# Kernel tuning notes

Hardware: AMD Instinct MI355X
Metric: run time of the kernel (lower is better)

The kernel has to match this reference:

```python
import jax, jax.numpy as jnp
import numpy as np

HEADS = 4  # from init_kwargs

def setup_inputs() -> dict:
    key = jax.random.key(0)
    ks = jax.random.split(key, 11)
    B, N, T, E = 1, 16, 2048, 64
    D = E // HEADS
    return {
        "value": jax.random.normal(ks[0], (B, N, T, E), jnp.float32),
        "key":   jax.random.normal(ks[1], (B, N, T, E), jnp.float32),
        "query": jax.random.normal(ks[2], (B, N, T, E), jnp.float32),
        "Wq": jax.random.normal(ks[3], (D, D), jnp.float32) / np.sqrt(D),
        "bq": jax.random.normal(ks[4], (D,), jnp.float32) * 0.01,
        "Wk": jax.random.normal(ks[5], (D, D), jnp.float32) / np.sqrt(D),
        "bk": jax.random.normal(ks[6], (D,), jnp.float32) * 0.01,
        "Wv": jax.random.normal(ks[7], (D, D), jnp.float32) / np.sqrt(D),
        "bv": jax.random.normal(ks[8], (D,), jnp.float32) * 0.01,
        "Wfc": jax.random.normal(ks[9], (E, E), jnp.float32) / np.sqrt(E),
        "bfc": jax.random.normal(ks[10], (E,), jnp.float32) * 0.01,
    }

def reference(value, key, query, Wq, bq, Wk, bk, Wv, bv, Wfc, bfc):
    B, N, T, E = query.shape
    H = HEADS
    D = E // H
    # split heads: [B,N,T,H,D]
    q = query.reshape(B, N, T, H, D) @ Wq + bq
    k = key.reshape(B, N, T, H, D) @ Wk + bk
    v = value.reshape(B, N, T, H, D) @ Wv + bv
    # full score tensor [B,N,Tq,Tk,H]
    scores = jnp.einsum('bnqhd,bnkhd->bnqkh', q, k)
    # NOTE: original softmaxes over dim=2, i.e. the QUERY axis (faithful to source)
    attn = jax.nn.softmax(scores / jnp.float32(E) ** 0.5, axis=2)
    out = jnp.einsum('bnqkh,bnkhd->bnqhd', attn, v).reshape(B, N, T, E)
    return out @ Wfc + bfc
```

## Files before the change

kernel.cpp:

```cpp
#include <hip/hip_runtime.h>

#define N_ 16
#define T_ 2048
#define E_ 64
#define H_ 4
#define D_ 16
#define NH_ 64
#define SEXP_ 0.18033688f

typedef __attribute__((ext_vector_type(4))) _Float16 h4;
typedef __attribute__((ext_vector_type(8))) _Float16 h8;
typedef __attribute__((ext_vector_type(2))) __fp16 g2;
typedef __attribute__((ext_vector_type(4))) float f4;

#if __has_builtin(__builtin_amdgcn_exp2f)
__device__ inline float fast_exp2(float x) { return __builtin_amdgcn_exp2f(x); }
#else
__device__ inline float fast_exp2(float x) {
    float r; asm("v_exp_f32 %0, %1" : "=v"(r) : "v"(x)); return r;
}
#endif

__device__ inline h4 pack4_f16(float a, float b, float c, float d) {
    union { g2 g[2]; h4 h; } u;
    u.g[0] = __builtin_amdgcn_cvt_pkrtz(a, b);
    u.g[1] = __builtin_amdgcn_cvt_pkrtz(c, d);
    return u.h;
}

__global__ __launch_bounds__(256) void proj_kernel(
    const float* __restrict__ xq, const float* __restrict__ Wq, const float* __restrict__ bq,
    const float* __restrict__ xk, const float* __restrict__ Wk, const float* __restrict__ bk,
    const float* __restrict__ xv, const float* __restrict__ Wv, const float* __restrict__ bv,
    const float* __restrict__ Wfc,
    _Float16* __restrict__ Qh, _Float16* __restrict__ Kh, _Float16* __restrict__ Vt,
    _Float16* __restrict__ Wt)
{
    int tid = threadIdx.x;
    int y = blockIdx.y;
    if (y == 3) {
        if (blockIdx.x < 16) {
            int k = blockIdx.x * 4 + (tid >> 6);
            int e = tid & 63;
            Wt[e * 64 + k] = (_Float16)Wfc[k * 64 + e];
        }
        return;
    }
    const float* x = (y == 0) ? xq : (y == 1) ? xk : xv;
    const float* W = (y == 0) ? Wq : (y == 1) ? Wk : Wv;
    const float* b = (y == 0) ? bq : (y == 1) ? bk : bv;
    const float sc = (y == 0) ? SEXP_ : 1.0f;

    __shared__ float Wl[D_ * D_];
    __shared__ float bl[D_];
    Wl[tid] = W[tid];
    if (tid < D_) bl[tid] = b[tid];
    __syncthreads();

    int r = blockIdx.x * 256 + tid;
    int h, t, n;
    if (y == 2) {
        t = r & (T_ - 1);
        h = (r >> 11) & (H_ - 1);
        n = r >> 13;
    } else {
        h = r & (H_ - 1);
        t = (r >> 2) & (T_ - 1);
        n = r >> 13;
    }

    const float4* xp4 = reinterpret_cast<const float4*>(
        x + ((size_t)(n * T_ + t) * E_ + h * D_));
    float xv_[D_];
#pragma unroll
    for (int i = 0; i < 4; i++) {
        float4 v = xp4[i];
        xv_[4*i] = v.x; xv_[4*i+1] = v.y; xv_[4*i+2] = v.z; xv_[4*i+3] = v.w;
    }
    float acc[D_];
#pragma unroll
    for (int i = 0; i < D_; i++) acc[i] = bl[i];
#pragma unroll
    for (int j = 0; j < D_; j++) {
        float xj = xv_[j];
#pragma unroll
        for (int i = 0; i < D_; i++) acc[i] = fmaf(xj, Wl[j * D_ + i], acc[i]);
    }
    if (y == 2) {
        _Float16* vb = Vt + (size_t)(n * H_ + h) * D_ * T_ + t;
#pragma unroll
        for (int d = 0; d < D_; d++) vb[(size_t)d * T_] = (_Float16)acc[d];
    } else {
        _Float16 ob[16];
#pragma unroll
        for (int i = 0; i < D_; i++) ob[i] = (_Float16)(acc[i] * sc);
        _Float16* out = (y == 0) ? Qh : Kh;
        uint4* dst = reinterpret_cast<uint4*>(out + (size_t)((n * H_ + h) * T_ + t) * D_);
        dst[0] = reinterpret_cast<uint4*>(ob)[0];
        dst[1] = reinterpret_cast<uint4*>(ob)[1];
    }
}

__global__ __launch_bounds__(256) void stats_kernel(
    const _Float16* __restrict__ Qh, const _Float16* __restrict__ Kh,
    float* __restrict__ Lp)
{
    int tid = threadIdx.x;
    int lane = tid & 63, wave = tid >> 6;
    int row = lane & 15, quad = lane >> 4;
    int nh = blockIdx.x;
    int kt0 = (blockIdx.y * 4 + wave) * 4;
    int z = blockIdx.z;
    const _Float16* Kb = Kh + (size_t)nh * T_ * D_;
    const _Float16* Qb = Qh + (size_t)nh * T_ * D_;

    h4 a[4];
#pragma unroll
    for (int j = 0; j < 4; j++)
        a[j] = *reinterpret_cast<const h4*>(Kb + ((kt0 + j) * 16 + row) * D_ + quad * 4);

    f4 l[4];
#pragma unroll
    for (int j = 0; j < 4; j++) l[j] = (f4){0.f, 0.f, 0.f, 0.f};
    f4 z4 = {0.f, 0.f, 0.f, 0.f};

    int q_lo = z * (T_ / 4), q_hi = q_lo + T_ / 4;
#pragma unroll 4
    for (int q0 = q_lo; q0 < q_hi; q0 += 16) {
        h4 b = *reinterpret_cast<const h4*>(Qb + (q0 + row) * D_ + quad * 4);
#pragma unroll
        for (int j = 0; j < 4; j++) {
            f4 s = __builtin_amdgcn_mfma_f32_16x16x16f16(a[j], b, z4, 0, 0, 0);
#pragma unroll
            for (int i = 0; i < 4; i++) l[j][i] += fast_exp2(s[i]);
        }
    }
#pragma unroll
    for (int off = 1; off < 16; off <<= 1)
#pragma unroll
        for (int j = 0; j < 4; j++)
#pragma unroll
            for (int i = 0; i < 4; i++)
                l[j][i] += __shfl_xor(l[j][i], off, 64);

    if (row == 0) {
        float* lp = Lp + ((size_t)z * NH_ + nh) * T_;
#pragma unroll
        for (int j = 0; j < 4; j++)
            *reinterpret_cast<f4*>(lp + (kt0 + j) * 16 + quad * 4) = l[j];
    }
}

__global__ __launch_bounds__(256) void combine_kernel(
    const float* __restrict__ Lp, _Float16* __restrict__ Vt)
{
    int nh = blockIdx.x >> 1;
    int k0 = (blockIdx.x & 1) * 1024 + threadIdx.x * 4;

    f4 s = {0.f, 0.f, 0.f, 0.f};
#pragma unroll
    for (int zz = 0; zz < 4; zz++) {
        f4 lv = *reinterpret_cast<const f4*>(Lp + ((size_t)zz * NH_ + nh) * T_ + k0);
        s[0] += lv[0]; s[1] += lv[1]; s[2] += lv[2]; s[3] += lv[3];
    }
    f4 r;
#pragma unroll
    for (int i = 0; i < 4; i++) r[i] = 1.0f / s[i];

    _Float16* vb = Vt + (size_t)nh * D_ * T_ + k0;
#pragma unroll
    for (int d = 0; d < D_; d++) {
        union { uint2 u; _Float16 hh[4]; } v;
        v.u = *reinterpret_cast<const uint2*>(vb + (size_t)d * T_);
        h4 sv = pack4_f16((float)v.hh[0] * r[0], (float)v.hh[1] * r[1],
                          (float)v.hh[2] * r[2], (float)v.hh[3] * r[3]);
        union { h4 h; uint2 u; } o; o.h = sv;
        *reinterpret_cast<uint2*>(vb + (size_t)d * T_) = o.u;
    }
}

__global__ __launch_bounds__(256) void attn_kernel(
    const _Float16* __restrict__ Qh, const _Float16* __restrict__ Kh,
    const _Float16* __restrict__ Vsc, float* __restrict__ PO)
{
    int tid = threadIdx.x;
    int lane = tid & 63, wave = tid >> 6;
    int row = lane & 15, quad = lane >> 4;
    int nh = blockIdx.x;
    int qt0 = (blockIdx.y * 4 + wave) * 4;
    int z = blockIdx.z;
    const _Float16* Kb = Kh + (size_t)nh * T_ * D_;
    const _Float16* Qb = Qh + (size_t)nh * T_ * D_;
    const _Float16* Vb = Vsc + (size_t)nh * D_ * T_ + (size_t)row * T_;

    h4 b[4];
#pragma unroll
    for (int j = 0; j < 4; j++)
        b[j] = *reinterpret_cast<const h4*>(Qb + ((qt0 + j) * 16 + row) * D_ + quad * 4);

    f4 o[4];
#pragma unroll
    for (int j = 0; j < 4; j++) o[j] = (f4){0.f, 0.f, 0.f, 0.f};
    f4 z4 = {0.f, 0.f, 0.f, 0.f};

    int pr = ((row & 12) << 1) | (row & 3);

    int k_lo = z * (T_ / 4), k_hi = k_lo + T_ / 4;
#pragma unroll 2
    for (int k0 = k_lo; k0 < k_hi; k0 += 32) {
        h4 a0 = *reinterpret_cast<const h4*>(Kb + (k0 + pr) * D_ + quad * 4);
        h4 a1 = *reinterpret_cast<const h4*>(Kb + (k0 + pr + 4) * D_ + quad * 4);
        h8 v = *reinterpret_cast<const h8*>(Vb + k0 + quad * 8);
#pragma unroll
        for (int j = 0; j < 4; j++) {
            f4 s0 = __builtin_amdgcn_mfma_f32_16x16x16f16(a0, b[j], z4, 0, 0, 0);
            f4 s1 = __builtin_amdgcn_mfma_f32_16x16x16f16(a1, b[j], z4, 0, 0, 0);
            union { h4 h[2]; h8 h8v; } p;
            p.h[0] = pack4_f16(fast_exp2(s0[0]), fast_exp2(s0[1]),
                               fast_exp2(s0[2]), fast_exp2(s0[3]));
            p.h[1] = pack4_f16(fast_exp2(s1[0]), fast_exp2(s1[1]),
                               fast_exp2(s1[2]), fast_exp2(s1[3]));
            o[j] = __builtin_amdgcn_mfma_f32_16x16x32_f16(p.h8v, v, o[j], 0, 0, 0);
        }
    }
    int n = nh >> 2, h = nh & 3;
    float* po = PO + (size_t)z * N_ * T_ * E_ + (size_t)n * T_ * E_ + h * D_ + row;
#pragma unroll
    for (int j = 0; j < 4; j++)
#pragma unroll
        for (int i = 0; i < 4; i++) {
            int q0 = (qt0 + j) * 16 + quad * 4 + i;
            po[(size_t)q0 * E_] = o[j][i];
        }
}

__global__ __launch_bounds__(256) void fc_kernel(
    const float* __restrict__ PO, const _Float16* __restrict__ Wt,
    const float* __restrict__ bfc, float* __restrict__ out)
{
    int tid = threadIdx.x;
    int lane = tid & 63, wave = tid >> 6;
    int row = lane & 15, quad = lane >> 4;
    int g = blockIdx.x * 4 + wave;
    int r0 = g * 16;

    size_t base = (size_t)(r0 + row) * E_;
    const size_t zstride = (size_t)N_ * T_ * E_ / 4;

    h8 a[2];
#pragma unroll
    for (int half = 0; half < 2; half++) {
        f4 u0 = {0.f,0.f,0.f,0.f}, u1 = {0.f,0.f,0.f,0.f};
#pragma unroll
        for (int zz = 0; zz < 4; zz++) {
            const f4* p = reinterpret_cast<const f4*>(PO) + zz * zstride + base / 4;
            f4 w0 = p[half * 8 + quad * 2];
            f4 w1 = p[half * 8 + quad * 2 + 1];
#pragma unroll
            for (int i = 0; i < 4; i++) { u0[i] += w0[i]; u1[i] += w1[i]; }
        }
        union { h4 h[2]; h8 v; } pk;
        pk.h[0] = pack4_f16(u0[0], u0[1], u0[2], u0[3]);
        pk.h[1] = pack4_f16(u1[0], u1[1], u1[2], u1[3]);
        a[half] = pk.v;
    }

    f4 acc[4];
#pragma unroll
    for (int ne = 0; ne < 4; ne++) {
        const _Float16* wtb = Wt + (size_t)(ne * 16 + row) * 64;
        h8 b0 = *reinterpret_cast<const h8*>(wtb + quad * 8);
        h8 b1 = *reinterpret_cast<const h8*>(wtb + 32 + quad * 8);
        acc[ne] = __builtin_amdgcn_mfma_f32_16x16x32_f16(a[0], b0, (f4){0.f,0.f,0.f,0.f}, 0, 0, 0);
        acc[ne] = __builtin_amdgcn_mfma_f32_16x16x32_f16(a[1], b1, acc[ne], 0, 0, 0);
    }
#pragma unroll
    for (int ne = 0; ne < 4; ne++) {
        float bias = bfc[ne * 16 + row];
#pragma unroll
        for (int i = 0; i < 4; i++)
            out[(size_t)(r0 + quad * 4 + i) * E_ + ne * 16 + row] = acc[ne][i] + bias;
    }
}

extern "C" void kernel_launch(void* const* d_in, const int* in_sizes, int n_in,
                              void* d_out, int out_size, void* d_ws, size_t ws_size,
                              hipStream_t stream) {
    (void)in_sizes; (void)n_in; (void)out_size; (void)ws_size;
    const float* value = (const float*)d_in[0];
    const float* key   = (const float*)d_in[1];
    const float* query = (const float*)d_in[2];
    const float* Wq    = (const float*)d_in[3];
    const float* bq    = (const float*)d_in[4];
    const float* Wk    = (const float*)d_in[5];
    const float* bk    = (const float*)d_in[6];
    const float* Wv    = (const float*)d_in[7];
    const float* bv    = (const float*)d_in[8];
    const float* Wfc   = (const float*)d_in[9];
    const float* bfc   = (const float*)d_in[10];
    float* out = (float*)d_out;

    char* ws = (char*)d_ws;
    _Float16* Qh  = (_Float16*)(ws);
    _Float16* Kh  = (_Float16*)(ws + (4u << 20));
    _Float16* Vt  = (_Float16*)(ws + (8u << 20));
    _Float16* Wt  = (_Float16*)(ws + (12u << 20));
    float*    Lp  = (float*)   (ws + (13u << 20));
    float*    PO  = (float*)   (ws + (15u << 20));

    proj_kernel<<<dim3(512, 4), 256, 0, stream>>>(
        query, Wq, bq, key, Wk, bk, value, Wv, bv, Wfc, Qh, Kh, Vt, Wt);
    stats_kernel<<<dim3(NH_, 8, 4), 256, 0, stream>>>(Qh, Kh, Lp);
    combine_kernel<<<128, 256, 0, stream>>>(Lp, Vt);
    attn_kernel<<<dim3(NH_, 8, 4), 256, 0, stream>>>(Qh, Kh, Vt, PO);
    fc_kernel<<<512, 256, 0, stream>>>(PO, Wt, bfc, out);
}
```

Measured before the change: 176.4 us.

## Fuse all stages into one cooperative kernel with grid-wide syncs

Replaces the five-kernel pipeline with a single cooperative mega-kernel of 1024 blocks that uses grid.sync between the projection, column-stats, attention and output-projection phases. It changes the split from 4 to 2 z-partitions, folds the reciprocal normalisation into an LDS table applied to V inside the attention loop, and drops the separate combine pass over V. The aim is to remove launch gaps and an extra read/write of V and partial sums. The cost is grid-barrier overhead and lower parallelism per phase, and it falls back to the old launches if the cooperative launch fails.

```diff
diff --git a/kernel.cpp b/kernel.cpp
--- a/kernel.cpp
+++ b/kernel.cpp
@@ -1,4 +1,7 @@
 #include <hip/hip_runtime.h>
+#include <hip/hip_cooperative_groups.h>
+
+namespace cg = cooperative_groups;
 
 #define N_ 16
 #define T_ 2048
@@ -26,6 +29,237 @@
     u.g[0] = __builtin_amdgcn_cvt_pkrtz(a, b);
     u.g[1] = __builtin_amdgcn_cvt_pkrtz(c, d);
     return u.h;
+}
+
+__global__ __launch_bounds__(256, 4) void mega_kernel(
+    const float* __restrict__ xq, const float* __restrict__ Wq, const float* __restrict__ bq,
+    const float* __restrict__ xk, const float* __restrict__ Wk, const float* __restrict__ bk,
+    const float* __restrict__ xv, const float* __restrict__ Wv, const float* __restrict__ bv,
+    const float* __restrict__ Wfc, const float* __restrict__ bfc,
+    _Float16* __restrict__ Qh, _Float16* __restrict__ Kh, _Float16* __restrict__ Vt,
+    _Float16* __restrict__ Wt, float* __restrict__ Lp, float* __restrict__ PO,
+    float* __restrict__ out)
+{
+    cg::grid_group grid = cg::this_grid();
+    int tid = threadIdx.x;
+    int lane = tid & 63, wave = tid >> 6;
+    int row = lane & 15, quad = lane >> 4;
+    int u = blockIdx.x;
+
+    __shared__ float Wl[D_ * D_];
+    __shared__ float bl[D_];
+    __shared__ __align__(16) _Float16 rlh[1024];
+
+    {
+        int y = u >> 8;
+        int x0 = (u & 255) * 2;
+        if (y == 3) {
+#pragma unroll
+            for (int xi = 0; xi < 2; xi++) {
+                int x = x0 + xi;
+                if (x < 16) {
+                    int k = x * 4 + (tid >> 6);
+                    int e = tid & 63;
+                    Wt[e * 64 + k] = (_Float16)Wfc[k * 64 + e];
+                }
+            }
+        } else {
+            const float* xx = (y == 0) ? xq : (y == 1) ? xk : xv;
+            const float* W  = (y == 0) ? Wq : (y == 1) ? Wk : Wv;
+            const float* b  = (y == 0) ? bq : (y == 1) ? bk : bv;
+            const float sc  = (y == 0) ? SEXP_ : 1.0f;
+
+            Wl[tid] = W[tid];
+            if (tid < D_) bl[tid] = b[tid];
+            __syncthreads();
+
+#pragma unroll
+            for (int xi = 0; xi < 2; xi++) {
+                int r = (x0 + xi) * 256 + tid;
+                int h, t, n;
+                if (y == 2) {
+                    t = r & (T_ - 1);
+                    h = (r >> 11) & (H_ - 1);
+                    n = r >> 13;
+                } else {
+                    h = r & (H_ - 1);
+                    t = (r >> 2) & (T_ - 1);
+                    n = r >> 13;
+                }
+                const float4* xp4 = reinterpret_cast<const float4*>(
+                    xx + ((size_t)(n * T_ + t) * E_ + h * D_));
+                float xv_[D_];
+#pragma unroll
+                for (int i = 0; i < 4; i++) {
+                    float4 v = xp4[i];
+                    xv_[4*i] = v.x; xv_[4*i+1] = v.y; xv_[4*i+2] = v.z; xv_[4*i+3] = v.w;
+                }
+                float acc[D_];
+#pragma unroll
+                for (int i = 0; i < D_; i++) acc[i] = bl[i];
+#pragma unroll
+                for (int j = 0; j < D_; j++) {
+                    float xj = xv_[j];
+#pragma unroll
+                    for (int i = 0; i < D_; i++) acc[i] = fmaf(xj, Wl[j * D_ + i], acc[i]);
+                }
+                if (y == 2) {
+                    _Float16* vb = Vt + (size_t)(n * H_ + h) * D_ * T_ + t;
+#pragma unroll
+                    for (int d = 0; d < D_; d++) vb[(size_t)d * T_] = (_Float16)acc[d];
+                } else {
+                    _Float16 ob[16];
+#pragma unroll
+                    for (int i = 0; i < D_; i++) ob[i] = (_Float16)(acc[i] * sc);
+                    _Float16* o = (y == 0) ? Qh : Kh;
+                    uint4* dst = reinterpret_cast<uint4*>(o + (size_t)((n * H_ + h) * T_ + t) * D_);
+                    dst[0] = reinterpret_cast<uint4*>(ob)[0];
+                    dst[1] = reinterpret_cast<uint4*>(ob)[1];
+                }
+            }
+        }
+    }
+    grid.sync();
+
+    {
+        int nh = u >> 4, y = (u >> 1) & 7, z = u & 1;
+        int kt0 = (y * 4 + wave) * 4;
+        const _Float16* Kb = Kh + (size_t)nh * T_ * D_;
+        const _Float16* Qb = Qh + (size_t)nh * T_ * D_;
+
+        h4 a[4];
+#pragma unroll
+        for (int j = 0; j < 4; j++)
+            a[j] = *reinterpret_cast<const h4*>(Kb + ((kt0 + j) * 16 + row) * D_ + quad * 4);
+
+        f4 l[4];
+#pragma unroll
+        for (int j = 0; j < 4; j++) l[j] = (f4){0.f, 0.f, 0.f, 0.f};
+        f4 z4 = {0.f, 0.f, 0.f, 0.f};
+
+        int q_lo = z * (T_ / 2), q_hi = q_lo + T_ / 2;
+#pragma unroll 4
+        for (int q0 = q_lo; q0 < q_hi; q0 += 16) {
+            h4 b = *reinterpret_cast<const h4*>(Qb + (q0 + row) * D_ + quad * 4);
+#pragma unroll
+            for (int j = 0; j < 4; j++) {
+                f4 s = __builtin_amdgcn_mfma_f32_16x16x16f16(a[j], b, z4, 0, 0, 0);
+#pragma unroll
+                for (int i = 0; i < 4; i++) l[j][i] += fast_exp2(s[i]);
+            }
+        }
+#pragma unroll
+        for (int off = 1; off < 16; off <<= 1)
+#pragma unroll
+            for (int j = 0; j < 4; j++)
+#pragma unroll
+                for (int i = 0; i < 4; i++)
+                    l[j][i] += __shfl_xor(l[j][i], off, 64);
+
+        if (row == 0) {
+            float* lp = Lp + ((size_t)z * NH_ + nh) * T_;
+#pragma unroll
+            for (int j = 0; j < 4; j++)
+                *reinterpret_cast<f4*>(lp + (kt0 + j) * 16 + quad * 4) = l[j];
+        }
+    }
+    grid.sync();
+
+    {
+        int nh = u >> 4, y = (u >> 1) & 7, z = u & 1;
+        int qt0 = (y * 4 + wave) * 4;
+        int k_lo = z * (T_ / 2);
+
+        {
+            int kk = tid * 4;
+            f4 s0 = *reinterpret_cast<const f4*>(Lp + (size_t)nh * T_ + k_lo + kk);
+            f4 s1 = *reinterpret_cast<const f4*>(Lp + ((size_t)NH_ + nh) * T_ + k_lo + kk);
+            h4 pk = pack4_f16(1.0f / (s0[0] + s1[0]), 1.0f / (s0[1] + s1[1]),
+                              1.0f / (s0[2] + s1[2]), 1.0f / (s0[3] + s1[3]));
+            *reinterpret_cast<h4*>(&rlh[kk]) = pk;
+        }
+        __syncthreads();
+
+        const _Float16* Kb = Kh + (size_t)nh * T_ * D_;
+        const _Float16* Qb = Qh + (size_t)nh * T_ * D_;
+        const _Float16* Vb = Vt + (size_t)nh * D_ * T_ + (size_t)row * T_;
+
+        h4 b[4];
+#pragma unroll
+        for (int j = 0; j < 4; j++)
+            b[j] = *reinterpret_cast<const h4*>(Qb + ((qt0 + j) * 16 + row) * D_ + quad * 4);
+
+        f4 o[4];
+#pragma unroll
+        for (int j = 0; j < 4; j++) o[j] = (f4){0.f, 0.f, 0.f, 0.f};
+        f4 z4 = {0.f, 0.f, 0.f, 0.f};
+
+        int pr = ((row & 12) << 1) | (row & 3);
+
+        int k_hi = k_lo + T_ / 2;
+#pragma unroll 2
+        for (int k0 = k_lo; k0 < k_hi; k0 += 32) {
+            h4 a0 = *reinterpret_cast<const h4*>(Kb + (k0 + pr) * D_ + quad * 4);
+            h4 a1 = *reinterpret_cast<const h4*>(Kb + (k0 + pr + 4) * D_ + quad * 4);
+            h8 v = *reinterpret_cast<const h8*>(Vb + k0 + quad * 8);
+            h8 rv = *reinterpret_cast<const h8*>(&rlh[(k0 - k_lo) + quad * 8]);
+            v = v * rv;
+#pragma unroll
+            for (int j = 0; j < 4; j++) {
+                f4 s0 = __builtin_amdgcn_mfma_f32_16x16x16f16(a0, b[j], z4, 0, 0, 0);
+                f4 s1 = __builtin_amdgcn_mfma_f32_16x16x16f16(a1, b[j], z4, 0, 0, 0);
+                union { h4 h[2]; h8 h8v; } p;
+                p.h[0] = pack4_f16(fast_exp2(s0[0]), fast_exp2(s0[1]),
+                                   fast_exp2(s0[2]), fast_exp2(s0[3]));
+                p.h[1] = pack4_f16(fast_exp2(s1[0]), fast_exp2(s1[1]),
+                                   fast_exp2(s1[2]), fast_exp2(s1[3]));
+                o[j] = __builtin_amdgcn_mfma_f32_16x16x32_f16(p.h8v, v, o[j], 0, 0, 0);
+            }
+        }
+        int n = nh >> 2, h = nh & 3;
+        float* po = PO + (size_t)z * N_ * T_ * E_ + (size_t)n * T_ * E_ + h * D_ + row;
+#pragma unroll
+        for (int j = 0; j < 4; j++)
+#pragma unroll
+            for (int i = 0; i < 4; i++) {
+                int q0 = (qt0 + j) * 16 + quad * 4 + i;
+                po[(size_t)q0 * E_] = o[j][i];
+            }
+    }
+    grid.sync();
+
+    {
+        const size_t zstride = (size_t)N_ * T_ * E_ / 4;
+        int ne = wave;
+#pragma unroll
+        for (int ti = 0; ti < 2; ti++) {
+            int r0 = (u * 2 + ti) * 16;
+            size_t base = (size_t)(r0 + row) * E_;
+
+            h8 a[2];
+#pragma unroll
+            for (int half = 0; half < 2; half++) {
+                const f4* p0 = reinterpret_cast<const f4*>(PO) + base / 4;
+                const f4* p1 = p0 + zstride;
+                f4 w0 = p0[half * 8 + quad * 2], w1 = p0[half * 8 + quad * 2 + 1];
+                f4 v0 = p1[half * 8 + quad * 2], v1 = p1[half * 8 + quad * 2 + 1];
+                union { h4 h[2]; h8 v; } pk;
+                pk.h[0] = pack4_f16(w0[0] + v0[0], w0[1] + v0[1], w0[2] + v0[2], w0[3] + v0[3]);
+                pk.h[1] = pack4_f16(w1[0] + v1[0], w1[1] + v1[1], w1[2] + v1[2], w1[3] + v1[3]);
+                a[half] = pk.v;
+            }
+            const _Float16* wtb = Wt + (size_t)(ne * 16 + row) * 64;
+            h8 b0 = *reinterpret_cast<const h8*>(wtb + quad * 8);
+            h8 b1 = *reinterpret_cast<const h8*>(wtb + 32 + quad * 8);
+            f4 acc = __builtin_amdgcn_mfma_f32_16x16x32_f16(a[0], b0, (f4){0.f,0.f,0.f,0.f}, 0, 0, 0);
+            acc = __builtin_amdgcn_mfma_f32_16x16x32_f16(a[1], b1, acc, 0, 0, 0);
+
+            float bias = bfc[ne * 16 + row];
+#pragma unroll
+            for (int i = 0; i < 4; i++)
+                out[(size_t)(r0 + quad * 4 + i) * E_ + ne * 16 + row] = acc[i] + bias;
+        }
+    }
 }
 
 __global__ __launch_bounds__(256) void proj_kernel(
@@ -68,7 +302,6 @@
         t = (r >> 2) & (T_ - 1);
         n = r >> 13;
     }
-
     const float4* xp4 = reinterpret_cast<const float4*>(
         x + ((size_t)(n * T_ + t) * E_ + h * D_));
     float xv_[D_];
@@ -94,8 +327,8 @@
         _Float16 ob[16];
 #pragma unroll
         for (int i = 0; i < D_; i++) ob[i] = (_Float16)(acc[i] * sc);
-        _Float16* out = (y == 0) ? Qh : Kh;
-        uint4* dst = reinterpret_cast<uint4*>(out + (size_t)((n * H_ + h) * T_ + t) * D_);
+        _Float16* o = (y == 0) ? Qh : Kh;
+        uint4* dst = reinterpret_cast<uint4*>(o + (size_t)((n * H_ + h) * T_ + t) * D_);
         dst[0] = reinterpret_cast<uint4*>(ob)[0];
         dst[1] = reinterpret_cast<uint4*>(ob)[1];
     }
@@ -118,7 +351,6 @@
 #pragma unroll
     for (int j = 0; j < 4; j++)
         a[j] = *reinterpret_cast<const h4*>(Kb + ((kt0 + j) * 16 + row) * D_ + quad * 4);
-
     f4 l[4];
 #pragma unroll
     for (int j = 0; j < 4; j++) l[j] = (f4){0.f, 0.f, 0.f, 0.f};
@@ -142,7 +374,6 @@
 #pragma unroll
             for (int i = 0; i < 4; i++)
                 l[j][i] += __shfl_xor(l[j][i], off, 64);
-
     if (row == 0) {
         float* lp = Lp + ((size_t)z * NH_ + nh) * T_;
 #pragma unroll
@@ -156,7 +387,6 @@
 {
     int nh = blockIdx.x >> 1;
     int k0 = (blockIdx.x & 1) * 1024 + threadIdx.x * 4;
-
     f4 s = {0.f, 0.f, 0.f, 0.f};
 #pragma unroll
     for (int zz = 0; zz < 4; zz++) {
@@ -166,7 +396,6 @@
     f4 r;
 #pragma unroll
     for (int i = 0; i < 4; i++) r[i] = 1.0f / s[i];
-
     _Float16* vb = Vt + (size_t)nh * D_ * T_ + k0;
 #pragma unroll
     for (int d = 0; d < D_; d++) {
@@ -197,12 +426,10 @@
 #pragma unroll
     for (int j = 0; j < 4; j++)
         b[j] = *reinterpret_cast<const h4*>(Qb + ((qt0 + j) * 16 + row) * D_ + quad * 4);
-
     f4 o[4];
 #pragma unroll
     for (int j = 0; j < 4; j++) o[j] = (f4){0.f, 0.f, 0.f, 0.f};
     f4 z4 = {0.f, 0.f, 0.f, 0.f};
-
     int pr = ((row & 12) << 1) | (row & 3);
 
     int k_lo = z * (T_ / 4), k_hi = k_lo + T_ / 4;
@@ -243,7 +470,6 @@
     int row = lane & 15, quad = lane >> 4;
     int g = blockIdx.x * 4 + wave;
     int r0 = g * 16;
-
     size_t base = (size_t)(r0 + row) * E_;
     const size_t zstride = (size_t)N_ * T_ * E_ / 4;
 
@@ -264,7 +490,6 @@
         pk.h[1] = pack4_f16(u1[0], u1[1], u1[2], u1[3]);
         a[half] = pk.v;
     }
-
     f4 acc[4];
 #pragma unroll
     for (int ne = 0; ne < 4; ne++) {
@@ -308,10 +533,17 @@
     float*    Lp  = (float*)   (ws + (13u << 20));
     float*    PO  = (float*)   (ws + (15u << 20));
 
-    proj_kernel<<<dim3(512, 4), 256, 0, stream>>>(
-        query, Wq, bq, key, Wk, bk, value, Wv, bv, Wfc, Qh, Kh, Vt, Wt);
-    stats_kernel<<<dim3(NH_, 8, 4), 256, 0, stream>>>(Qh, Kh, Lp);
-    combine_kernel<<<128, 256, 0, stream>>>(Lp, Vt);
-    attn_kernel<<<dim3(NH_, 8, 4), 256, 0, stream>>>(Qh, Kh, Vt, PO);
-    fc_kernel<<<512, 256, 0, stream>>>(PO, Wt, bfc, out);
-}
+    void* args[] = { &query, &Wq, &bq, &key, &Wk, &bk, &value, &Wv, &bv,
+                     &Wfc, &bfc, &Qh, &Kh, &Vt, &Wt, &Lp, &PO, &out };
+    hipError_t err = hipLaunchCooperativeKernel(
+        reinterpret_cast<void*>(mega_kernel), dim3(1024), dim3(256), args, 0, stream);
+    if (err != hipSuccess) {
+        (void)hipGetLastError();
+        proj_kernel<<<dim3(512, 4), 256, 0, stream>>>(
+            query, Wq, bq, key, Wk, bk, value, Wv, bv, Wfc, Qh, Kh, Vt, Wt);
+        stats_kernel<<<dim3(NH_, 8, 4), 256, 0, stream>>>(Qh, Kh, Lp);
+        combine_kernel<<<128, 256, 0, stream>>>(Lp, Vt);
+        attn_kernel<<<dim3(NH_, 8, 4), 256, 0, stream>>>(Qh, Kh, Vt, PO);
+        fc_kernel<<<512, 256, 0, stream>>>(PO, Wt, bfc, out);
+    }
+}
```

New measurement: 532.5 us. 3.02x slower.

## Fuse softmax normalization into attention kernel and restructure inner loops

Applied to the files above, without the earlier changes.

Removes the separate combine kernel. Each attention block now sums the four partial softmax denominators for its key chunk, stores the reciprocals as fp16 in shared memory, and scales V by them inside the main loop. Both stats and attention loops are rewritten with pointer increments and fixed inner unrolls, and launch bounds now request 8 blocks per CU. This saves one kernel launch and a read-modify-write pass over V, but adds redundant reciprocal work per block and an extra fp16 multiply per V load.

```diff
diff --git a/kernel.cpp b/kernel.cpp
--- a/kernel.cpp
+++ b/kernel.cpp
@@ -94,14 +94,14 @@
         _Float16 ob[16];
 #pragma unroll
         for (int i = 0; i < D_; i++) ob[i] = (_Float16)(acc[i] * sc);
-        _Float16* out = (y == 0) ? Qh : Kh;
-        uint4* dst = reinterpret_cast<uint4*>(out + (size_t)((n * H_ + h) * T_ + t) * D_);
+        _Float16* o = (y == 0) ? Qh : Kh;
+        uint4* dst = reinterpret_cast<uint4*>(o + (size_t)((n * H_ + h) * T_ + t) * D_);
         dst[0] = reinterpret_cast<uint4*>(ob)[0];
         dst[1] = reinterpret_cast<uint4*>(ob)[1];
     }
 }
 
-__global__ __launch_bounds__(256) void stats_kernel(
+__global__ __launch_bounds__(256, 8) void stats_kernel(
     const _Float16* __restrict__ Qh, const _Float16* __restrict__ Kh,
     float* __restrict__ Lp)
 {
@@ -124,16 +124,20 @@
     for (int j = 0; j < 4; j++) l[j] = (f4){0.f, 0.f, 0.f, 0.f};
     f4 z4 = {0.f, 0.f, 0.f, 0.f};
 
-    int q_lo = z * (T_ / 4), q_hi = q_lo + T_ / 4;
-#pragma unroll 4
-    for (int q0 = q_lo; q0 < q_hi; q0 += 16) {
-        h4 b = *reinterpret_cast<const h4*>(Qb + (q0 + row) * D_ + quad * 4);
-#pragma unroll
-        for (int j = 0; j < 4; j++) {
-            f4 s = __builtin_amdgcn_mfma_f32_16x16x16f16(a[j], b, z4, 0, 0, 0);
-#pragma unroll
-            for (int i = 0; i < 4; i++) l[j][i] += fast_exp2(s[i]);
-        }
+    int q_lo = z * (T_ / 4);
+    const _Float16* qp = Qb + (size_t)(q_lo + row) * D_ + quad * 4;
+    for (int it = 0; it < (T_ / 4) / 64; it++) {
+#pragma unroll
+        for (int m = 0; m < 4; m++) {
+            h4 b = *reinterpret_cast<const h4*>(qp + m * 16 * D_);
+#pragma unroll
+            for (int j = 0; j < 4; j++) {
+                f4 s = __builtin_amdgcn_mfma_f32_16x16x16f16(a[j], b, z4, 0, 0, 0);
+#pragma unroll
+                for (int i = 0; i < 4; i++) l[j][i] += fast_exp2(s[i]);
+            }
+        }
+        qp += 64 * D_;
     }
 #pragma unroll
     for (int off = 1; off < 16; off <<= 1)
@@ -151,47 +155,37 @@
     }
 }
 
-__global__ __launch_bounds__(256) void combine_kernel(
-    const float* __restrict__ Lp, _Float16* __restrict__ Vt)
+__global__ __launch_bounds__(256, 8) void attn_kernel(
+    const _Float16* __restrict__ Qh, const _Float16* __restrict__ Kh,
+    const _Float16* __restrict__ Vt, const float* __restrict__ Lp,
+    float* __restrict__ PO)
 {
-    int nh = blockIdx.x >> 1;
-    int k0 = (blockIdx.x & 1) * 1024 + threadIdx.x * 4;
-
-    f4 s = {0.f, 0.f, 0.f, 0.f};
-#pragma unroll
-    for (int zz = 0; zz < 4; zz++) {
-        f4 lv = *reinterpret_cast<const f4*>(Lp + ((size_t)zz * NH_ + nh) * T_ + k0);
-        s[0] += lv[0]; s[1] += lv[1]; s[2] += lv[2]; s[3] += lv[3];
-    }
-    f4 r;
-#pragma unroll
-    for (int i = 0; i < 4; i++) r[i] = 1.0f / s[i];
-
-    _Float16* vb = Vt + (size_t)nh * D_ * T_ + k0;
-#pragma unroll
-    for (int d = 0; d < D_; d++) {
-        union { uint2 u; _Float16 hh[4]; } v;
-        v.u = *reinterpret_cast<const uint2*>(vb + (size_t)d * T_);
-        h4 sv = pack4_f16((float)v.hh[0] * r[0], (float)v.hh[1] * r[1],
-                          (float)v.hh[2] * r[2], (float)v.hh[3] * r[3]);
-        union { h4 h; uint2 u; } o; o.h = sv;
-        *reinterpret_cast<uint2*>(vb + (size_t)d * T_) = o.u;
-    }
-}
-
-__global__ __launch_bounds__(256) void attn_kernel(
-    const _Float16* __restrict__ Qh, const _Float16* __restrict__ Kh,
-    const _Float16* __restrict__ Vsc, float* __restrict__ PO)
-{
+    __shared__ __align__(16) _Float16 rlh[512];
     int tid = threadIdx.x;
     int lane = tid & 63, wave = tid >> 6;
     int row = lane & 15, quad = lane >> 4;
     int nh = blockIdx.x;
     int qt0 = (blockIdx.y * 4 + wave) * 4;
     int z = blockIdx.z;
+    int k_lo = z * (T_ / 4);
+
+    {
+        int kk = tid * 2;
+        float s0 = 0.f, s1 = 0.f;
+#pragma unroll
+        for (int zz = 0; zz < 4; zz++) {
+            float2 lv = *reinterpret_cast<const float2*>(
+                Lp + ((size_t)zz * NH_ + nh) * T_ + k_lo + kk);
+            s0 += lv.x; s1 += lv.y;
+        }
+        g2 pk = __builtin_amdgcn_cvt_pkrtz(1.0f / s0, 1.0f / s1);
+        *reinterpret_cast<g2*>(&rlh[kk]) = pk;
+    }
+    __syncthreads();
+
     const _Float16* Kb = Kh + (size_t)nh * T_ * D_;
     const _Float16* Qb = Qh + (size_t)nh * T_ * D_;
-    const _Float16* Vb = Vsc + (size_t)nh * D_ * T_ + (size_t)row * T_;
+    const _Float16* Vb = Vt + (size_t)nh * D_ * T_ + (size_t)row * T_;
 
     h4 b[4];
 #pragma unroll
@@ -205,23 +199,32 @@
 
     int pr = ((row & 12) << 1) | (row & 3);
 
-    int k_lo = z * (T_ / 4), k_hi = k_lo + T_ / 4;
-#pragma unroll 2
-    for (int k0 = k_lo; k0 < k_hi; k0 += 32) {
-        h4 a0 = *reinterpret_cast<const h4*>(Kb + (k0 + pr) * D_ + quad * 4);
-        h4 a1 = *reinterpret_cast<const h4*>(Kb + (k0 + pr + 4) * D_ + quad * 4);
-        h8 v = *reinterpret_cast<const h8*>(Vb + k0 + quad * 8);
-#pragma unroll
-        for (int j = 0; j < 4; j++) {
-            f4 s0 = __builtin_amdgcn_mfma_f32_16x16x16f16(a0, b[j], z4, 0, 0, 0);
-            f4 s1 = __builtin_amdgcn_mfma_f32_16x16x16f16(a1, b[j], z4, 0, 0, 0);
-            union { h4 h[2]; h8 h8v; } p;
-            p.h[0] = pack4_f16(fast_exp2(s0[0]), fast_exp2(s0[1]),
-                               fast_exp2(s0[2]), fast_exp2(s0[3]));
-            p.h[1] = pack4_f16(fast_exp2(s1[0]), fast_exp2(s1[1]),
-                               fast_exp2(s1[2]), fast_exp2(s1[3]));
-            o[j] = __builtin_amdgcn_mfma_f32_16x16x32_f16(p.h8v, v, o[j], 0, 0, 0);
-        }
+    const _Float16* kp = Kb + (size_t)(k_lo + pr) * D_ + quad * 4;
+    const _Float16* vp = Vb + k_lo + quad * 8;
+    const _Float16* rp = rlh + quad * 8;
+    for (int it = 0; it < (T_ / 4) / 128; it++) {
+#pragma unroll
+        for (int m = 0; m < 4; m++) {
+            h4 a0 = *reinterpret_cast<const h4*>(kp + m * 32 * D_);
+            h4 a1 = *reinterpret_cast<const h4*>(kp + m * 32 * D_ + 4 * D_);
+            h8 v = *reinterpret_cast<const h8*>(vp + m * 32);
+            h8 rv = *reinterpret_cast<const h8*>(rp + m * 32);
+            v = v * rv;
+#pragma unroll
+            for (int j = 0; j < 4; j++) {
+                f4 s0 = __builtin_amdgcn_mfma_f32_16x16x16f16(a0, b[j], z4, 0, 0, 0);
+                f4 s1 = __builtin_amdgcn_mfma_f32_16x16x16f16(a1, b[j], z4, 0, 0, 0);
+                union { h4 h[2]; h8 h8v; } p;
+                p.h[0] = pack4_f16(fast_exp2(s0[0]), fast_exp2(s0[1]),
+                                   fast_exp2(s0[2]), fast_exp2(s0[3]));
+                p.h[1] = pack4_f16(fast_exp2(s1[0]), fast_exp2(s1[1]),
+                                   fast_exp2(s1[2]), fast_exp2(s1[3]));
+                o[j] = __builtin_amdgcn_mfma_f32_16x16x32_f16(p.h8v, v, o[j], 0, 0, 0);
+            }
+        }
+        kp += 128 * D_;
+        vp += 128;
+        rp += 128;
     }
     int n = nh >> 2, h = nh & 3;
     float* po = PO + (size_t)z * N_ * T_ * E_ + (size_t)n * T_ * E_ + h * D_ + row;
@@ -243,7 +246,6 @@
     int row = lane & 15, quad = lane >> 4;
     int g = blockIdx.x * 4 + wave;
     int r0 = g * 16;
-
     size_t base = (size_t)(r0 + row) * E_;
     const size_t zstride = (size_t)N_ * T_ * E_ / 4;
 
@@ -264,7 +266,6 @@
         pk.h[1] = pack4_f16(u1[0], u1[1], u1[2], u1[3]);
         a[half] = pk.v;
     }
-
     f4 acc[4];
 #pragma unroll
     for (int ne = 0; ne < 4; ne++) {
@@ -311,7 +312,6 @@
     proj_kernel<<<dim3(512, 4), 256, 0, stream>>>(
         query, Wq, bq, key, Wk, bk, value, Wv, bv, Wfc, Qh, Kh, Vt, Wt);
     stats_kernel<<<dim3(NH_, 8, 4), 256, 0, stream>>>(Qh, Kh, Lp);
-    combine_kernel<<<128, 256, 0, stream>>>(Lp, Vt);
-    attn_kernel<<<dim3(NH_, 8, 4), 256, 0, stream>>>(Qh, Kh, Vt, PO);
+    attn_kernel<<<dim3(NH_, 8, 4), 256, 0, stream>>>(Qh, Kh, Vt, Lp, PO);
     fc_kernel<<<512, 256, 0, stream>>>(PO, Wt, bfc, out);
 }
```

New measurement: 229.2 us. 1.3x slower.
